# Kernel optimization log

Hardware: AMD Instinct MI355X
Metric: run time of the kernel (lower is better)

Reference implementation:

```python
import jax, jax.numpy as jnp
import numpy as np
from jax import lax

CUTOFF = 0.25
SIGMA = 1.0
RADIUS = 4  # skimage/scipy default truncate=4.0 -> radius = round(4.0*sigma)


def _gauss_kernel(sigma=SIGMA, radius=RADIUS):
    x = np.arange(-radius, radius + 1, dtype=np.float32)
    k = np.exp(-0.5 * (x / sigma) ** 2)
    return jnp.asarray(k / k.sum())


def _blur_axis(x, axis, kernel):
    r = (kernel.shape[0] - 1) // 2
    pad = [(0, 0)] * x.ndim
    pad[axis] = (r, r)
    xp = jnp.pad(x, pad, mode='edge')  # scipy mode='nearest'
    out = jnp.zeros_like(x)
    for i in range(kernel.shape[0]):  # fixed small tap loop (9 taps)
        out = out + kernel[i] * lax.slice_in_dim(xp, i, i + x.shape[axis], axis=axis)
    return out


def gaussian_smoothing_4d(x):
    # skimage.filters.gaussian on a 4D array smooths over ALL axes (B, C, H, W)
    k = _gauss_kernel().astype(x.dtype)
    for ax in range(4):
        x = _blur_axis(x, ax, k)
    return x


def dht_2d(x):
    # real(FFT(x)) - imag(FFT(flip(x)))
    return (jnp.fft.fftn(x, axes=(2, 3)).real
            - jnp.fft.fftn(jnp.flip(x, axis=(2, 3)), axes=(2, 3)).imag).astype(x.dtype)


def _neg_k(a):
    # X_H(-k): flip both spatial mode axes, then roll by 1 (DC stays put)
    return jnp.roll(jnp.flip(a, axis=(-2, -1)), shift=(1, 1), axis=(-2, -1))


def compl_mul2d(x1, x2):
    x1n, x2n = _neg_k(x1), _neg_k(x2)
    e = lambda a, b: jnp.einsum('bixy,ioxy->boxy', a, b)
    return 0.5 * (e(x1, x2) - e(x1n, x2n) + e(x1, x2n) + e(x1n, x2))


def setup_inputs() -> dict:
    key = jax.random.key(0)
    k1, k2 = jax.random.split(key)
    B, Cin, Cout, H, W, M1, M2 = 16, 64, 64, 128, 128, 20, 20
    x = jax.random.normal(k1, (B, Cin, H, W), dtype=jnp.float32)
    scale = 1.0 / (Cin * Cout)
    w1 = scale * jax.random.uniform(k2, (Cin, Cout, M1, M2), dtype=jnp.float32)
    return {'x': x, 'w1': w1}


def reference(x, w1):
    B, _, H, W = x.shape
    Cout, M1, M2 = w1.shape[1], w1.shape[2], w1.shape[3]
    x_ht = dht_2d(x)
    out_ht = jnp.zeros((B, Cout, H, W), dtype=x.dtype)
    out_ht = out_ht.at[:, :, :M1, :M2].set(
        compl_mul2d(x_ht[:, :, :M1, :M2], w1))
    # inverse DHT = DHT / (H*W)
    y = dht_2d(out_ht) / (H * W)
    y = gaussian_smoothing_4d(y)
    # low-pass mask along last dim only (as in the original)
    freqs = jnp.fft.fftfreq(W)
    mask = (jnp.abs(freqs) <= CUTOFF).astype(y.dtype)
    return y * mask
```

## Files before the change

kernel.cpp:

```cpp
#include <hip/hip_runtime.h>


#define TWO_PI 6.283185307179586f
#define THETA (TWO_PI / 128.0f)

__device__ __forceinline__ void gauss9(float* g) {
  float s = 0.f;
#pragma unroll
  for (int t = 0; t < 9; ++t) { float d = (float)(t - 4); g[t] = expf(-0.5f * d * d); s += g[t]; }
  float inv = 1.f / s;
#pragma unroll
  for (int t = 0; t < 9; ++t) g[t] *= inv;
}

__global__ void kA_init(float* __restrict__ L2g, float* __restrict__ RB2g,
                        float* __restrict__ Tg, float* __restrict__ Lf2g,
                        const float* __restrict__ w1, float* __restrict__ wbT) {
  __shared__ float sh[5632];
  int tid = threadIdx.x;
  int blk = blockIdx.x;
  if (blk == 1) {
    for (int i = tid; i < 5120; i += 256) {
      int n2 = i / 40, col = i - n2 * 40;
      int k2 = (col < 20) ? col : col - 20;
      float a = (float)((k2 * n2) & 127) * THETA;
      Tg[i] = (col < 20) ? cosf(a) : sinf(a);
    }
    return;
  }
  if (blk == 2) {
    for (int i = tid; i < 10240; i += 256) {
      int k1 = i >> 9, t = i & 511;
      int q = t >> 7, n1 = t & 127;
      int nn = n1 + ((q >= 2) ? 1 : 0);
      float a = (float)((k1 * nn) & 127) * THETA;
      float v;
      if (q == 0) v = cosf(a);
      else if (q == 1) v = -sinf(a);
      else if (q == 2) v = -sinf(a);
      else v = -cosf(a);
      Lf2g[i] = v;
    }
    return;
  }
  if (blk == 0) {
    for (int i = tid; i < 5376; i += 256) {
      int u = i / 42, t = i - u * 42;
      int A = (t < 21) ? t : t - 21;
      float a = (float)((u * A) & 127) * THETA;
      sh[u * 44 + t] = (t < 21) ? cosf(a) : sinf(a);
    }
    __syncthreads();
    float g[9]; gauss9(g);
    for (int i = tid; i < 5376; i += 256) {
      int u = i / 42, t = i - u * 42;
      float acc = 0.f;
#pragma unroll
      for (int tp = 0; tp < 9; ++tp) {
        int uc = u - 4 + tp; uc = uc < 0 ? 0 : (uc > 127 ? 127 : uc);
        acc += g[tp] * sh[uc * 44 + t];
      }
      L2g[t * 128 + u] = acc;
      bool keep = (u <= 32) || (u >= 96);
      RB2g[t * 128 + u] = keep ? acc : 0.f;
    }
    return;
  }
  int bb = blk - 3;
  int c = bb / 7, chunk = bb % 7;
  int m0 = chunk * 64;
  int mw = 400 - m0; if (mw > 64) mw = 64;
  for (int t = tid; t < 4096; t += 256) {
    int o = t >> 6, mm = t & 63;
    sh[o * 69 + mm] = (mm < mw) ? w1[(c * 64 + o) * 400 + m0 + mm] : 0.f;
  }
  __syncthreads();
  float g[9]; gauss9(g);
  for (int t = tid; t < 4096; t += 256) {
    int mm = t >> 6, o = t & 63;
    if (mm >= mw) continue;
    float acc = 0.f;
#pragma unroll
    for (int tp = 0; tp < 9; ++tp) {
      int oc = o - 4 + tp; oc = oc < 0 ? 0 : (oc > 63 ? 63 : oc);
      acc += g[tp] * sh[oc * 69 + mm];
    }
    wbT[(c * 400 + m0 + mm) * 64 + o] = acc;
  }
}

__global__ void __launch_bounds__(320, 6) k12(const float* __restrict__ x,
                                              const float* __restrict__ Tg,
                                              const float* __restrict__ Lf2g,
                                              float* __restrict__ X1) {
  __shared__ float lds[5120];
  int bc = blockIdx.x, tid = threadIdx.x;
  int w = __builtin_amdgcn_readfirstlane(tid >> 6);
  int L = tid & 63;
  const float* xb = x + (long)bc * 16384;
  const float* tgw = Tg + w * 8;

  float acc[2][8];
#pragma unroll
  for (int i = 0; i < 2; ++i)
#pragma unroll
    for (int j = 0; j < 8; ++j) acc[i][j] = 0.f;

  for (int ch = 0; ch < 4; ++ch) {
    __syncthreads();
    for (int t = tid; t < 1024; t += 320) {
      int n2l = t & 31, n1g = t >> 5;
      const float* gp = xb + n1g * 512 + ch * 32 + n2l;
      float4 v = make_float4(gp[0], gp[128], gp[256], gp[384]);
      *(float4*)&lds[n2l * 132 + n1g * 4] = v;
    }
    __syncthreads();
#pragma unroll 4
    for (int k = 0; k < 32; ++k) {
      float2 av = *(const float2*)&lds[k * 132 + 2 * L];
      const float* tr = tgw + (ch * 32 + k) * 40;
      float4 b0 = *(const float4*)tr;
      float4 b1 = *(const float4*)(tr + 4);
      float bv[8] = {b0.x, b0.y, b0.z, b0.w, b1.x, b1.y, b1.z, b1.w};
#pragma unroll
      for (int j = 0; j < 8; ++j) {
        acc[0][j] += av.x * bv[j];
        acc[1][j] += av.y * bv[j];
      }
    }
  }
  __syncthreads();
#pragma unroll
  for (int j = 0; j < 8; ++j) {
    int col = w * 8 + j;
    int k2 = (col < 20) ? col : col - 20;
    int part = (col < 20) ? 0 : 128;
    int m = (k2 & 7) << 2;
    *(float2*)&lds[k2 * 256 + ((part + 2 * L) ^ m)] =
        make_float2(acc[0][j], acc[1][j]);
  }
  __syncthreads();
  if (tid < 200) {
    int k1 = tid / 10, k2 = (tid % 10) * 2;
    int m0 = (k2 & 7) << 2, m1 = ((k2 + 1) & 7) << 2;
    const float* lrow = Lf2g + k1 * 512;
    const float* p0 = lds + k2 * 256;
    const float* p1 = lds + (k2 + 1) * 256;
    float d0a = 0.f, d1a = 0.f, d2ca = 0.f, d2sa = 0.f, d3ca = 0.f, d3sa = 0.f;
    float d0b = 0.f, d1b = 0.f, d2cb = 0.f, d2sb = 0.f, d3cb = 0.f, d3sb = 0.f;
    for (int t = 0; t < 128; t += 4) {
      float4 l0 = *(const float4*)(lrow + t);
      float4 l1 = *(const float4*)(lrow + 128 + t);
      float4 l2 = *(const float4*)(lrow + 256 + t);
      float4 l3 = *(const float4*)(lrow + 384 + t);
      float4 pc0 = *(const float4*)(p0 + (t ^ m0));
      float4 ps0 = *(const float4*)(p0 + ((128 + t) ^ m0));
      float4 pc1 = *(const float4*)(p1 + (t ^ m1));
      float4 ps1 = *(const float4*)(p1 + ((128 + t) ^ m1));
      d0a += l0.x*pc0.x + l0.y*pc0.y + l0.z*pc0.z + l0.w*pc0.w;
      d1a += l1.x*ps0.x + l1.y*ps0.y + l1.z*ps0.z + l1.w*ps0.w;
      d2ca += l2.x*pc0.x + l2.y*pc0.y + l2.z*pc0.z + l2.w*pc0.w;
      d2sa += l2.x*ps0.x + l2.y*ps0.y + l2.z*ps0.z + l2.w*ps0.w;
      d3ca += l3.x*pc0.x + l3.y*pc0.y + l3.z*pc0.z + l3.w*pc0.w;
      d3sa += l3.x*ps0.x + l3.y*ps0.y + l3.z*ps0.z + l3.w*ps0.w;
      d0b += l0.x*pc1.x + l0.y*pc1.y + l0.z*pc1.z + l0.w*pc1.w;
      d1b += l1.x*ps1.x + l1.y*ps1.y + l1.z*ps1.z + l1.w*ps1.w;
      d2cb += l2.x*pc1.x + l2.y*pc1.y + l2.z*pc1.z + l2.w*pc1.w;
      d2sb += l2.x*ps1.x + l2.y*ps1.y + l2.z*ps1.z + l2.w*ps1.w;
      d3cb += l3.x*pc1.x + l3.y*pc1.y + l3.z*pc1.z + l3.w*pc1.w;
      d3sb += l3.x*ps1.x + l3.y*ps1.y + l3.z*ps1.z + l3.w*ps1.w;
    }
    float ska, cka, skb, ckb;
    sincosf(THETA * (float)k2, &ska, &cka);
    sincosf(THETA * (float)(k2 + 1), &skb, &ckb);
    X1[(k1 * 20 + k2) * 1024 + bc] = d0a + d1a + cka * (d2ca + d3sa) + ska * (d3ca - d2sa);
    X1[(k1 * 20 + k2 + 1) * 1024 + bc] = d0b + d1b + ckb * (d2cb + d3sb) + skb * (d3cb - d2sb);
  }
}

__global__ void k3_mix(const float* __restrict__ X1, const float* __restrict__ wbT,
                       float* __restrict__ O) {
  __shared__ float Xp[4][64], Xm[4][64];
  int m = blockIdx.x >> 2, bq = blockIdx.x & 3;
  int i = m / 20, j = m - i * 20;
  int nm = ((20 - i) % 20) * 20 + ((20 - j) % 20);
  int tid = threadIdx.x;
  const float sc = 0.5f / 16384.0f;
  float g[9]; gauss9(g);
  {
    int bl = tid >> 6, c = tid & 63;
    int b = bq * 4 + bl;
    float sa = 0.f, sn = 0.f;
#pragma unroll
    for (int tp = 0; tp < 9; ++tp) {
      int bb = b - 4 + tp; bb = bb < 0 ? 0 : (bb > 15 ? 15 : bb);
      sa += g[tp] * X1[m * 1024 + bb * 64 + c];
      sn += g[tp] * X1[nm * 1024 + bb * 64 + c];
    }
    Xp[bl][c] = (sa + sn) * sc; Xm[bl][c] = (sa - sn) * sc;
  }
  __syncthreads();
  int o = tid & 63, bl = tid >> 6;
  int b = bq * 4 + bl;
  float acc = 0.f;
#pragma unroll 4
  for (int c = 0; c < 64; ++c) {
    acc += wbT[(c * 400 + m) * 64 + o] * Xp[bl][c]
         + wbT[(c * 400 + nm) * 64 + o] * Xm[bl][c];
  }
  O[(b * 64 + o) * 400 + m] = acc;
}

__global__ void __launch_bounds__(256) k5b_final(const float* __restrict__ O,
                                                 const float* __restrict__ L2g,
                                                 const float* __restrict__ RB2g,
                                                 float* __restrict__ out) {
  __shared__ float Os[400];
  __shared__ float Rs[42 * 128];
  int bo = blockIdx.x, tid = threadIdx.x;
  for (int t = tid; t < 400; t += 256) Os[t] = O[bo * 400 + t];
  __syncthreads();
  const float4* Bc4 = (const float4*)RB2g;
  const float4* Bs4 = (const float4*)(RB2g + 21 * 128);
  {
    int vq = tid & 31, rg = tid >> 5;
    if (rg < 7) {
      int r0 = rg * 6;
      float4 a[6];
#pragma unroll
      for (int i = 0; i < 6; ++i) a[i] = make_float4(0.f, 0.f, 0.f, 0.f);
      for (int k2 = 0; k2 <= 20; ++k2) {
        float4 bc = Bc4[k2 * 32 + vq];
        float4 bs = Bs4[k2 * 32 + vq];
#pragma unroll
        for (int i = 0; i < 6; ++i) {
          int r = r0 + i;
          bool isS = (r >= 21);
          int A = isS ? (r - 21) : r;
          if (k2 < 20 && A < 20) {
            float ov = Os[A * 20 + k2];
            const float4 b = isS ? bs : bc;
            float s = isS ? -ov : ov;
            a[i].x += s * b.x; a[i].y += s * b.y; a[i].z += s * b.z; a[i].w += s * b.w;
          }
          if (k2 >= 1 && A >= 1) {
            float ov = Os[(A - 1) * 20 + (k2 - 1)];
            const float4 b = isS ? bc : bs;
            a[i].x -= ov * b.x; a[i].y -= ov * b.y; a[i].z -= ov * b.z; a[i].w -= ov * b.w;
          }
        }
      }
#pragma unroll
      for (int i = 0; i < 6; ++i)
        *(float4*)&Rs[(r0 + i) * 128 + vq * 4] = a[i];
    }
  }
  __syncthreads();
  int ug = tid >> 4, vg = tid & 15;
  int u0 = ug * 8, v0 = vg * 4;
  float acc[8][8];
#pragma unroll
  for (int i = 0; i < 8; ++i)
#pragma unroll
    for (int j = 0; j < 8; ++j) acc[i][j] = 0.f;
  for (int r = 0; r < 42; ++r) {
    float4 a0 = *(const float4*)(L2g + r * 128 + u0);
    float4 a1 = *(const float4*)(L2g + r * 128 + u0 + 4);
    float4 b0 = *(const float4*)&Rs[r * 128 + v0];
    float4 b1 = *(const float4*)&Rs[r * 128 + 64 + v0];
    float av[8] = {a0.x, a0.y, a0.z, a0.w, a1.x, a1.y, a1.z, a1.w};
    float bv[8] = {b0.x, b0.y, b0.z, b0.w, b1.x, b1.y, b1.z, b1.w};
#pragma unroll
    for (int i = 0; i < 8; ++i)
#pragma unroll
      for (int j = 0; j < 8; ++j) acc[i][j] += av[i] * bv[j];
  }
  long base = (long)bo * 16384;
#pragma unroll
  for (int i = 0; i < 8; ++i) {
    float4 s0 = make_float4(acc[i][0], acc[i][1], acc[i][2], acc[i][3]);
    float4 s1 = make_float4(acc[i][4], acc[i][5], acc[i][6], acc[i][7]);
    *(float4*)&out[base + (u0 + i) * 128 + v0] = s0;
    *(float4*)&out[base + (u0 + i) * 128 + 64 + v0] = s1;
  }
}

extern "C" void kernel_launch(void* const* d_in, const int* in_sizes, int n_in,
                              void* d_out, int out_size, void* d_ws, size_t ws_size,
                              hipStream_t stream) {
  const float* x = (const float*)d_in[0];
  const float* w1 = (const float*)d_in[1];
  float* out = (float*)d_out;
  float* ws = (float*)d_ws;

  float* X1 = ws;
  float* O = X1 + 409600;
  float* wbT = O + 409600;
  float* Tg = wbT + 1638400;
  float* Lf2g = Tg + 5120;
  float* L2g = Lf2g + 10240;
  float* RB2g = L2g + 5376;

  hipLaunchKernelGGL(kA_init, dim3(451), dim3(256), 0, stream,
                     L2g, RB2g, Tg, Lf2g, w1, wbT);
  hipLaunchKernelGGL(k12, dim3(1024), dim3(320), 0, stream, x, Tg, Lf2g, X1);
  hipLaunchKernelGGL(k3_mix, dim3(1600), dim3(256), 0, stream, X1, wbT, O);
  hipLaunchKernelGGL(k5b_final, dim3(1024), dim3(256), 0, stream, O, L2g, RB2g, out);
}
```

Before: 197.1 us.

## Skip masked output columns, prefetch k12 input in halves, batch k3 over all b

Result: slower. 208.4 us (+5.7%).

```diff
diff --git a/kernel.cpp b/kernel.cpp
--- a/kernel.cpp
+++ b/kernel.cpp
@@ -89,11 +89,11 @@
   }
 }
 
-__global__ void __launch_bounds__(320, 6) k12(const float* __restrict__ x,
+__global__ void __launch_bounds__(320, 5) k12(const float* __restrict__ x,
                                               const float* __restrict__ Tg,
                                               const float* __restrict__ Lf2g,
                                               float* __restrict__ X1) {
-  __shared__ float lds[5120];
+  __shared__ float lds[8448];
   int bc = blockIdx.x, tid = threadIdx.x;
   int w = __builtin_amdgcn_readfirstlane(tid >> 6);
   int L = tid & 63;
@@ -106,19 +106,42 @@
 #pragma unroll
     for (int j = 0; j < 8; ++j) acc[i][j] = 0.f;
 
-  for (int ch = 0; ch < 4; ++ch) {
+  float4 pv[7];
+#pragma unroll
+  for (int i = 0; i < 7; ++i) {
+    int t = tid + 320 * i;
+    if (t < 2048) {
+      int n2l = t & 63, n1g = t >> 6;
+      const float* gp = xb + n1g * 512 + n2l;
+      pv[i] = make_float4(gp[0], gp[128], gp[256], gp[384]);
+    }
+  }
+  for (int ch = 0; ch < 2; ++ch) {
     __syncthreads();
-    for (int t = tid; t < 1024; t += 320) {
-      int n2l = t & 31, n1g = t >> 5;
-      const float* gp = xb + n1g * 512 + ch * 32 + n2l;
-      float4 v = make_float4(gp[0], gp[128], gp[256], gp[384]);
-      *(float4*)&lds[n2l * 132 + n1g * 4] = v;
+#pragma unroll
+    for (int i = 0; i < 7; ++i) {
+      int t = tid + 320 * i;
+      if (t < 2048) {
+        int n2l = t & 63, n1g = t >> 6;
+        *(float4*)&lds[n2l * 132 + n1g * 4] = pv[i];
+      }
+    }
+    if (ch == 0) {
+#pragma unroll
+      for (int i = 0; i < 7; ++i) {
+        int t = tid + 320 * i;
+        if (t < 2048) {
+          int n2l = t & 63, n1g = t >> 6;
+          const float* gp = xb + n1g * 512 + 64 + n2l;
+          pv[i] = make_float4(gp[0], gp[128], gp[256], gp[384]);
+        }
+      }
     }
     __syncthreads();
 #pragma unroll 4
-    for (int k = 0; k < 32; ++k) {
+    for (int k = 0; k < 64; ++k) {
       float2 av = *(const float2*)&lds[k * 132 + 2 * L];
-      const float* tr = tgw + (ch * 32 + k) * 40;
+      const float* tr = tgw + (ch * 64 + k) * 40;
       float4 b0 = *(const float4*)tr;
       float4 b1 = *(const float4*)(tr + 4);
       float bv[8] = {b0.x, b0.y, b0.z, b0.w, b1.x, b1.y, b1.z, b1.w};
@@ -180,8 +203,8 @@
 
 __global__ void k3_mix(const float* __restrict__ X1, const float* __restrict__ wbT,
                        float* __restrict__ O) {
-  __shared__ float Xp[4][64], Xm[4][64];
-  int m = blockIdx.x >> 2, bq = blockIdx.x & 3;
+  __shared__ float Xp[16][64], Xm[16][64];
+  int m = blockIdx.x;
   int i = m / 20, j = m - i * 20;
   int nm = ((20 - i) % 20) * 20 + ((20 - j) % 20);
   int tid = threadIdx.x;
@@ -189,26 +212,33 @@
   float g[9]; gauss9(g);
   {
     int bl = tid >> 6, c = tid & 63;
-    int b = bq * 4 + bl;
-    float sa = 0.f, sn = 0.f;
-#pragma unroll
-    for (int tp = 0; tp < 9; ++tp) {
-      int bb = b - 4 + tp; bb = bb < 0 ? 0 : (bb > 15 ? 15 : bb);
-      sa += g[tp] * X1[m * 1024 + bb * 64 + c];
-      sn += g[tp] * X1[nm * 1024 + bb * 64 + c];
-    }
-    Xp[bl][c] = (sa + sn) * sc; Xm[bl][c] = (sa - sn) * sc;
-  }
-  __syncthreads();
-  int o = tid & 63, bl = tid >> 6;
-  int b = bq * 4 + bl;
-  float acc = 0.f;
+#pragma unroll
+    for (int it = 0; it < 4; ++it) {
+      int b = bl * 4 + it;
+      float sa = 0.f, sn = 0.f;
+#pragma unroll
+      for (int tp = 0; tp < 9; ++tp) {
+        int bb = b - 4 + tp; bb = bb < 0 ? 0 : (bb > 15 ? 15 : bb);
+        sa += g[tp] * X1[m * 1024 + bb * 64 + c];
+        sn += g[tp] * X1[nm * 1024 + bb * 64 + c];
+      }
+      Xp[b][c] = (sa + sn) * sc; Xm[b][c] = (sa - sn) * sc;
+    }
+  }
+  __syncthreads();
+  int o = tid & 63, bq = tid >> 6;
+  float acc[4] = {0.f, 0.f, 0.f, 0.f};
 #pragma unroll 4
   for (int c = 0; c < 64; ++c) {
-    acc += wbT[(c * 400 + m) * 64 + o] * Xp[bl][c]
-         + wbT[(c * 400 + nm) * 64 + o] * Xm[bl][c];
-  }
-  O[(b * 64 + o) * 400 + m] = acc;
+    float wp = wbT[(c * 400 + m) * 64 + o];
+    float wm = wbT[(c * 400 + nm) * 64 + o];
+#pragma unroll
+    for (int k = 0; k < 4; ++k)
+      acc[k] += Xp[bq * 4 + k][c] * wp + Xm[bq * 4 + k][c] * wm;
+  }
+#pragma unroll
+  for (int k = 0; k < 4; ++k)
+    O[((bq * 4 + k) * 64 + o) * 400 + m] = acc[k];
 }
 
 __global__ void __launch_bounds__(256) k5b_final(const float* __restrict__ O,
@@ -223,65 +253,78 @@
   const float4* Bc4 = (const float4*)RB2g;
   const float4* Bs4 = (const float4*)(RB2g + 21 * 128);
   {
-    int vq = tid & 31, rg = tid >> 5;
-    if (rg < 7) {
+    int rg = tid & 7;
+    int vqIdx = tid >> 3;
+    int vq = (vqIdx < 9) ? vqIdx : vqIdx + 15;
+    if (rg < 7 && vqIdx < 17) {
       int r0 = rg * 6;
       float4 a[6];
 #pragma unroll
-      for (int i = 0; i < 6; ++i) a[i] = make_float4(0.f, 0.f, 0.f, 0.f);
+      for (int q = 0; q < 6; ++q) a[q] = make_float4(0.f, 0.f, 0.f, 0.f);
       for (int k2 = 0; k2 <= 20; ++k2) {
         float4 bc = Bc4[k2 * 32 + vq];
         float4 bs = Bs4[k2 * 32 + vq];
 #pragma unroll
-        for (int i = 0; i < 6; ++i) {
-          int r = r0 + i;
+        for (int q = 0; q < 6; ++q) {
+          int r = r0 + q;
           bool isS = (r >= 21);
           int A = isS ? (r - 21) : r;
           if (k2 < 20 && A < 20) {
             float ov = Os[A * 20 + k2];
             const float4 b = isS ? bs : bc;
             float s = isS ? -ov : ov;
-            a[i].x += s * b.x; a[i].y += s * b.y; a[i].z += s * b.z; a[i].w += s * b.w;
+            a[q].x += s * b.x; a[q].y += s * b.y; a[q].z += s * b.z; a[q].w += s * b.w;
           }
           if (k2 >= 1 && A >= 1) {
             float ov = Os[(A - 1) * 20 + (k2 - 1)];
             const float4 b = isS ? bc : bs;
-            a[i].x -= ov * b.x; a[i].y -= ov * b.y; a[i].z -= ov * b.z; a[i].w -= ov * b.w;
+            a[q].x -= ov * b.x; a[q].y -= ov * b.y; a[q].z -= ov * b.z; a[q].w -= ov * b.w;
           }
         }
       }
 #pragma unroll
-      for (int i = 0; i < 6; ++i)
-        *(float4*)&Rs[(r0 + i) * 128 + vq * 4] = a[i];
-    }
-  }
-  __syncthreads();
-  int ug = tid >> 4, vg = tid & 15;
-  int u0 = ug * 8, v0 = vg * 4;
-  float acc[8][8];
-#pragma unroll
-  for (int i = 0; i < 8; ++i)
-#pragma unroll
-    for (int j = 0; j < 8; ++j) acc[i][j] = 0.f;
-  for (int r = 0; r < 42; ++r) {
-    float4 a0 = *(const float4*)(L2g + r * 128 + u0);
-    float4 a1 = *(const float4*)(L2g + r * 128 + u0 + 4);
-    float4 b0 = *(const float4*)&Rs[r * 128 + v0];
-    float4 b1 = *(const float4*)&Rs[r * 128 + 64 + v0];
-    float av[8] = {a0.x, a0.y, a0.z, a0.w, a1.x, a1.y, a1.z, a1.w};
-    float bv[8] = {b0.x, b0.y, b0.z, b0.w, b1.x, b1.y, b1.z, b1.w};
-#pragma unroll
-    for (int i = 0; i < 8; ++i)
-#pragma unroll
-      for (int j = 0; j < 8; ++j) acc[i][j] += av[i] * bv[j];
-  }
+      for (int q = 0; q < 6; ++q)
+        *(float4*)&Rs[(r0 + q) * 128 + vq * 4] = a[q];
+    }
+  }
+  __syncthreads();
   long base = (long)bo * 16384;
-#pragma unroll
-  for (int i = 0; i < 8; ++i) {
-    float4 s0 = make_float4(acc[i][0], acc[i][1], acc[i][2], acc[i][3]);
-    float4 s1 = make_float4(acc[i][4], acc[i][5], acc[i][6], acc[i][7]);
-    *(float4*)&out[base + (u0 + i) * 128 + v0] = s0;
-    *(float4*)&out[base + (u0 + i) * 128 + 64 + v0] = s1;
+  {
+    int half = tid >> 7;
+    int uu = (tid >> 3) & 15;  int u0 = uu * 8;
+    int vv = tid & 7;          int v0 = half ? (96 + vv * 4) : vv * 4;
+    float acc[8][4];
+#pragma unroll
+    for (int a = 0; a < 8; ++a)
+#pragma unroll
+      for (int b = 0; b < 4; ++b) acc[a][b] = 0.f;
+    for (int r = 0; r < 42; ++r) {
+      float4 a0 = *(const float4*)(L2g + r * 128 + u0);
+      float4 a1 = *(const float4*)(L2g + r * 128 + u0 + 4);
+      float4 b0 = *(const float4*)&Rs[r * 128 + v0];
+      float av[8] = {a0.x, a0.y, a0.z, a0.w, a1.x, a1.y, a1.z, a1.w};
+      float bv[4] = {b0.x, b0.y, b0.z, b0.w};
+#pragma unroll
+      for (int a = 0; a < 8; ++a)
+#pragma unroll
+        for (int b = 0; b < 4; ++b) acc[a][b] += av[a] * bv[b];
+    }
+#pragma unroll
+    for (int a = 0; a < 8; ++a)
+      *(float4*)&out[base + (u0 + a) * 128 + v0] =
+          make_float4(acc[a][0], acc[a][1], acc[a][2], acc[a][3]);
+  }
+  if (tid < 128) {
+    float d = 0.f;
+    for (int r = 0; r < 42; ++r) d += L2g[r * 128 + tid] * Rs[r * 128 + 32];
+    out[base + tid * 128 + 32] = d;
+  }
+  float4 z4 = make_float4(0.f, 0.f, 0.f, 0.f);
+  for (int jj = tid; jj < 2048; jj += 256) {
+    int u = jj >> 4, s = jj & 15;
+    long p = base + (long)u * 128;
+    if (s == 15) { out[p + 33] = 0.f; out[p + 34] = 0.f; out[p + 35] = 0.f; }
+    else *(float4*)&out[p + 36 + 4 * s] = z4;
   }
 }
 
@@ -304,6 +347,6 @@
   hipLaunchKernelGGL(kA_init, dim3(451), dim3(256), 0, stream,
                      L2g, RB2g, Tg, Lf2g, w1, wbT);
   hipLaunchKernelGGL(k12, dim3(1024), dim3(320), 0, stream, x, Tg, Lf2g, X1);
-  hipLaunchKernelGGL(k3_mix, dim3(1600), dim3(256), 0, stream, X1, wbT, O);
+  hipLaunchKernelGGL(k3_mix, dim3(400), dim3(256), 0, stream, X1, wbT, O);
   hipLaunchKernelGGL(k5b_final, dim3(1024), dim3(256), 0, stream, O, L2g, RB2g, out);
 }
```
